# Performance work log

Measured on AMD Instinct MI355X. Metric: run time of the kernel, lower is better.

## Reference

```python
import jax, jax.numpy as jnp
import numpy as np

WS = 8       # window_size
SHIFT = 4    # shift_size
NH = 6       # num_heads
C = 192      # dim
EPS = 1e-5


def _rel_index(ws):
    # standard Swin relative position index, [ws*ws, ws*ws]
    coords = np.stack(np.meshgrid(np.arange(ws), np.arange(ws), indexing='ij')).reshape(2, -1)
    rel = coords[:, :, None] - coords[:, None, :]            # [2, N, N]
    rel = rel.transpose(1, 2, 0) + (ws - 1)                  # shift to >= 0
    return rel[..., 0] * (2 * ws - 1) + rel[..., 1]          # [N, N]


def _attn_mask(h, w, ws, shift):
    # shifted-window attention mask, [nW, N, N] with 0 / -100
    img = np.zeros((h, w), dtype=np.float32)
    cnt = 0
    for hs in (slice(0, -ws), slice(-ws, -shift), slice(-shift, None)):
        for wsl in (slice(0, -ws), slice(-ws, -shift), slice(-shift, None)):
            img[hs, wsl] = cnt
            cnt += 1
    mw = img.reshape(h // ws, ws, w // ws, ws).transpose(0, 2, 1, 3).reshape(-1, ws * ws)
    diff = mw[:, None, :] - mw[:, :, None]
    return np.where(diff != 0, -100.0, 0.0).astype(np.float32)


def _ln(x, g, b):
    m = x.mean(-1, keepdims=True)
    v = ((x - m) ** 2).mean(-1, keepdims=True)
    return (x - m) / jnp.sqrt(v + EPS) * g + b


def setup_inputs() -> dict:
    key = jax.random.key(0)
    ks = jax.random.split(key, 16)
    B, H, W = 32, 64, 64
    Ch = 4 * C
    s = 0.02
    return {
        'x': jax.random.normal(ks[0], (B, H * W, C), jnp.float32),
        'h': H,
        'w': W,
        'norm1_g': jnp.ones((C,), jnp.float32),
        'norm1_b': jnp.zeros((C,), jnp.float32),
        'qkv_w': jax.random.normal(ks[1], (3 * C, C), jnp.float32) * s,
        'qkv_b': jnp.zeros((3 * C,), jnp.float32),
        'rpb_table': jax.random.normal(ks[2], ((2 * WS - 1) ** 2, NH), jnp.float32) * s,
        'proj_w': jax.random.normal(ks[3], (C, C), jnp.float32) * s,
        'proj_b': jnp.zeros((C,), jnp.float32),
        'norm2_g': jnp.ones((C,), jnp.float32),
        'norm2_b': jnp.zeros((C,), jnp.float32),
        'fc1_w': jax.random.normal(ks[4], (Ch, C), jnp.float32) * s,
        'fc1_b': jnp.zeros((Ch,), jnp.float32),
        'fc2_w': jax.random.normal(ks[5], (C, Ch), jnp.float32) * s,
        'fc2_b': jnp.zeros((C,), jnp.float32),
    }


def reference(x, h, w, norm1_g, norm1_b, qkv_w, qkv_b, rpb_table, proj_w, proj_b,
              norm2_g, norm2_b, fc1_w, fc1_b, fc2_w, fc2_b):
    B, L, _ = x.shape
    N = WS * WS
    hd = C // NH
    scale = hd ** -0.5
    nW = (h // WS) * (w // WS)

    shortcut = x
    xn = _ln(x, norm1_g, norm1_b).reshape(B, h, w, C)
    xs = jnp.roll(xn, (-SHIFT, -SHIFT), (1, 2))
    # window partition -> [B*nW, N, C]
    xw = xs.reshape(B, h // WS, WS, w // WS, WS, C).transpose(0, 1, 3, 2, 4, 5).reshape(-1, N, C)

    qkv = (xw @ qkv_w.T + qkv_b).reshape(-1, N, 3, NH, hd).transpose(2, 0, 3, 1, 4)
    q, k, v = qkv[0], qkv[1], qkv[2]                          # [B*nW, NH, N, hd]
    attn = jnp.einsum('whnd,whmd->whnm', q * scale, k)        # [B*nW, NH, N, N]
    bias = rpb_table[jnp.asarray(_rel_index(WS))].transpose(2, 0, 1)  # [NH, N, N]
    attn = attn + bias[None]
    mask = jnp.asarray(_attn_mask(h, w, WS, SHIFT))           # [nW, N, N]
    attn = attn.reshape(B, nW, NH, N, N) + mask[None, :, None]
    attn = jax.nn.softmax(attn.reshape(-1, NH, N, N), axis=-1)
    out = jnp.einsum('whnm,whmd->whnd', attn, v).transpose(0, 2, 1, 3).reshape(-1, N, C)
    out = out @ proj_w.T + proj_b

    # window reverse + unroll
    out = out.reshape(B, h // WS, w // WS, WS, WS, C).transpose(0, 1, 3, 2, 4, 5).reshape(B, h, w, C)
    out = jnp.roll(out, (SHIFT, SHIFT), (1, 2)).reshape(B, h * w, C)

    x = shortcut + out
    xn = _ln(x, norm2_g, norm2_b)
    mlp = jax.nn.gelu(xn @ fc1_w.T + fc1_b, approximate=False) @ fc2_w.T + fc2_b
    return x + mlp
```

## Files before the change

### kernel.cpp

```cpp
#include <hip/hip_runtime.h>
#include <hip/hip_bf16.h>
#include <math.h>

typedef __bf16 bf16;
typedef __bf16 bf16x8 __attribute__((ext_vector_type(8)));
typedef float f32x4 __attribute__((ext_vector_type(4)));

typedef const __attribute__((address_space(1))) char gchar;
typedef __attribute__((address_space(3))) char lchar;

#define BATCH 32
#define HW 64
#define L 4096
#define CDIM 192
#define NHEADS 6
#define HD 32
#define NTOK 131072
#define QKVC 576
#define CH 768

template <bool PERM, typename TIN>
__global__ __launch_bounds__(256) void ln_kernel(const TIN* __restrict__ xin,
                                                 const float* __restrict__ g,
                                                 const float* __restrict__ bta,
                                                 bf16* __restrict__ yout) {
  int wave = threadIdx.x >> 6;
  int lane = threadIdx.x & 63;
  int tok = blockIdx.x * 4 + wave;
  int src;
  if (PERM) {
    int win = tok >> 6;
    int n = tok & 63;
    int bb = win >> 6;
    int wid = win & 63;
    int i = ((wid >> 3) << 3) + (n >> 3);
    int j = ((wid & 7) << 3) + (n & 7);
    int sh = (i + 4) & 63;
    int sw = (j + 4) & 63;
    src = bb * L + sh * HW + sw;
  } else {
    src = tok;
  }
  const TIN* sp = xin + (size_t)src * CDIM;
  float v0 = (float)sp[lane];
  float v1 = (float)sp[lane + 64];
  float v2 = (float)sp[lane + 128];
  float s = v0 + v1 + v2;
#pragma unroll
  for (int off = 32; off; off >>= 1) s += __shfl_xor(s, off, 64);
  float mean = s * (1.0f / 192.0f);
  float d0 = v0 - mean, d1 = v1 - mean, d2 = v2 - mean;
  float q = d0 * d0 + d1 * d1 + d2 * d2;
#pragma unroll
  for (int off = 32; off; off >>= 1) q += __shfl_xor(q, off, 64);
  float rstd = rsqrtf(q * (1.0f / 192.0f) + 1e-5f);
  bf16* dp = yout + (size_t)tok * CDIM;
  dp[lane]       = (bf16)(d0 * rstd * g[lane]       + bta[lane]);
  dp[lane + 64]  = (bf16)(d1 * rstd * g[lane + 64]  + bta[lane + 64]);
  dp[lane + 128] = (bf16)(d2 * rstd * g[lane + 128] + bta[lane + 128]);
}

template <int EPI, typename TR, typename TO>
__global__ __launch_bounds__(256) void gemm_bt(const bf16* __restrict__ A,
                                               const float* __restrict__ W,
                                               const float* __restrict__ bias,
                                               const TR* __restrict__ res,
                                               TO* __restrict__ Cout,
                                               int M, int N, int K, int ldw) {
  __shared__ alignas(16) bf16 As[128 * 32];
  __shared__ alignas(16) bf16 Bs[64 * 32];
  const int gx = gridDim.x;
  const int nb = gx * gridDim.y;
  const int id = blockIdx.y * gx + blockIdx.x;
  const int per = nb >> 3;
  const int jj = ((id & 7) * per) + (id >> 3);
  const int n0 = (jj % gx) * 64;
  const int m0 = (jj / gx) * 128;
  const int tid = threadIdx.x;
  const int lane = tid & 63;
  const int wave = tid >> 6;
  const int wm = (wave >> 1) * 64;
  const int wn = (wave & 1) * 32;
  const int lr = lane & 15;
  const int quad = lane >> 4;

  f32x4 acc[4][2];
#pragma unroll
  for (int i = 0; i < 4; i++)
#pragma unroll
    for (int j = 0; j < 2; j++) acc[i][j] = (f32x4){0.f, 0.f, 0.f, 0.f};

  const int arow = tid >> 2;
  const int akq = (tid & 3) * 8;

  for (int k0 = 0; k0 < K; k0 += 32) {
    const bf16* Ap = A + (size_t)(m0 + arow) * K + k0 + akq;
    *(uint4*)(&As[arow * 32 + akq]) = *(const uint4*)Ap;
    *(uint4*)(&As[(arow + 64) * 32 + akq]) = *(const uint4*)(Ap + (size_t)64 * K);
    const float* Wp = W + (size_t)(n0 + arow) * ldw + k0 + akq;
    float4 w0 = *(const float4*)Wp;
    float4 w1 = *(const float4*)(Wp + 4);
    bf16x8 bw;
    bw[0] = (bf16)w0.x; bw[1] = (bf16)w0.y; bw[2] = (bf16)w0.z; bw[3] = (bf16)w0.w;
    bw[4] = (bf16)w1.x; bw[5] = (bf16)w1.y; bw[6] = (bf16)w1.z; bw[7] = (bf16)w1.w;
    *(bf16x8*)(&Bs[arow * 32 + akq]) = bw;
    __syncthreads();

    bf16x8 af[4], bfr[2];
#pragma unroll
    for (int mi = 0; mi < 4; mi++)
      af[mi] = *(const bf16x8*)(&As[(wm + mi * 16 + lr) * 32 + quad * 8]);
#pragma unroll
    for (int nj = 0; nj < 2; nj++)
      bfr[nj] = *(const bf16x8*)(&Bs[(wn + nj * 16 + lr) * 32 + quad * 8]);
#pragma unroll
    for (int mi = 0; mi < 4; mi++)
#pragma unroll
      for (int nj = 0; nj < 2; nj++)
        acc[mi][nj] = __builtin_amdgcn_mfma_f32_16x16x32_bf16(af[mi], bfr[nj],
                                                              acc[mi][nj], 0, 0, 0);
    __syncthreads();
  }

#pragma unroll
  for (int mi = 0; mi < 4; mi++) {
#pragma unroll
    for (int nj = 0; nj < 2; nj++) {
      int col = n0 + wn + nj * 16 + lr;
      float bv = bias[col];
#pragma unroll
      for (int r = 0; r < 4; r++) {
        int row = m0 + wm + mi * 16 + quad * 4 + r;
        float v = acc[mi][nj][r] + bv;
        size_t didx;
        if (EPI == 3) {
          int win = row >> 6, n = row & 63;
          int bb = win >> 6, wid = win & 63;
          int i = ((wid >> 3) << 3) + (n >> 3);
          int j = ((wid & 7) << 3) + (n & 7);
          int fi = (i + 4) & 63;
          int fj = (j + 4) & 63;
          didx = ((size_t)(bb * L + fi * HW + fj)) * (size_t)N + col;
          v += (float)res[didx];
        } else {
          didx = (size_t)row * N + col;
        }
        Cout[didx] = (TO)v;
      }
    }
  }
}

__device__ __forceinline__ int region64(int h) {
  return (h < 56) ? 0 : ((h < 60) ? 1 : 2);
}

__global__ __launch_bounds__(64) void attn_kernel(const bf16* __restrict__ qkv,
                                                  const float* __restrict__ rpb,
                                                  bf16* __restrict__ out) {
  __shared__ alignas(16) bf16 QKP[64 * 64];
  __shared__ alignas(16) bf16 Vt[32 * 64];
  bf16* Qs = QKP;
  bf16* Ks = QKP + 64 * 32;
  bf16* Ps = QKP;
  const int win = blockIdx.x;
  const int head = blockIdx.y;
  const int lane = threadIdx.x;
  const int lr = lane & 15;
  const int quad = lane >> 4;
  const int wid = win & 63;
  const int wi = wid >> 3, wj = wid & 7;

  const bf16* base = qkv + (size_t)win * 64 * QKVC + head * HD;
#pragma unroll
  for (int rep = 0; rep < 4; rep++) {
    int r = (lane >> 2) + rep * 16;
    int c = (lane & 3) * 8;
    *(uint4*)(&Qs[r * 32 + c]) = *(const uint4*)(base + (size_t)r * QKVC + c);
    *(uint4*)(&Ks[r * 32 + c]) = *(const uint4*)(base + CDIM + (size_t)r * QKVC + c);
    uint4 vv = *(const uint4*)(base + 2 * CDIM + (size_t)r * QKVC + c);
    bf16x8 v8 = __builtin_bit_cast(bf16x8, vv);
#pragma unroll
    for (int j = 0; j < 8; j++) Vt[(c + j) * 64 + r] = v8[j];
  }
  __syncthreads();

  f32x4 s[4][4];
  {
    bf16x8 qf[4], kf[4];
#pragma unroll
    for (int mi = 0; mi < 4; mi++)
      qf[mi] = *(const bf16x8*)(&Qs[(mi * 16 + lr) * 32 + quad * 8]);
#pragma unroll
    for (int nj = 0; nj < 4; nj++)
      kf[nj] = *(const bf16x8*)(&Ks[(nj * 16 + lr) * 32 + quad * 8]);
#pragma unroll
    for (int mi = 0; mi < 4; mi++)
#pragma unroll
      for (int nj = 0; nj < 4; nj++)
        s[mi][nj] = __builtin_amdgcn_mfma_f32_16x16x32_bf16(
            qf[mi], kf[nj], (f32x4){0.f, 0.f, 0.f, 0.f}, 0, 0, 0);
  }

  const float scale = 0.17677669529663687f;
#pragma unroll
  for (int mi = 0; mi < 4; mi++) {
#pragma unroll
    for (int nj = 0; nj < 4; nj++) {
#pragma unroll
      for (int r = 0; r < 4; r++) {
        int rr = mi * 16 + quad * 4 + r;
        int cc = nj * 16 + lr;
        int qi = rr >> 3, qj = rr & 7, ki = cc >> 3, kj = cc & 7;
        int idx = (qi - ki + 7) * 15 + (qj - kj + 7);
        float bv = rpb[idx * NHEADS + head];
        int regr = 3 * region64(wi * 8 + qi) + region64(wj * 8 + qj);
        int regc = 3 * region64(wi * 8 + ki) + region64(wj * 8 + kj);
        float mv = (regr != regc) ? -100.0f : 0.0f;
        s[mi][nj][r] = s[mi][nj][r] * scale + bv + mv;
      }
    }
  }

#pragma unroll
  for (int mi = 0; mi < 4; mi++) {
#pragma unroll
    for (int r = 0; r < 4; r++) {
      float mx = s[mi][0][r];
#pragma unroll
      for (int nj = 1; nj < 4; nj++) mx = fmaxf(mx, s[mi][nj][r]);
#pragma unroll
      for (int off = 1; off < 16; off <<= 1) mx = fmaxf(mx, __shfl_xor(mx, off, 64));
      float sum = 0.f;
#pragma unroll
      for (int nj = 0; nj < 4; nj++) {
        float p = __expf(s[mi][nj][r] - mx);
        s[mi][nj][r] = p;
        sum += p;
      }
#pragma unroll
      for (int off = 1; off < 16; off <<= 1) sum += __shfl_xor(sum, off, 64);
      float inv = 1.0f / sum;
#pragma unroll
      for (int nj = 0; nj < 4; nj++) s[mi][nj][r] *= inv;
    }
  }

#pragma unroll
  for (int mi = 0; mi < 4; mi++)
#pragma unroll
    for (int nj = 0; nj < 4; nj++)
#pragma unroll
      for (int r = 0; r < 4; r++)
        Ps[(mi * 16 + quad * 4 + r) * 64 + nj * 16 + lr] = (bf16)s[mi][nj][r];
  __syncthreads();

  f32x4 o[4][2];
#pragma unroll
  for (int mi = 0; mi < 4; mi++)
#pragma unroll
    for (int nj = 0; nj < 2; nj++) o[mi][nj] = (f32x4){0.f, 0.f, 0.f, 0.f};
#pragma unroll
  for (int ks = 0; ks < 2; ks++) {
    bf16x8 pf[4], vf[2];
#pragma unroll
    for (int mi = 0; mi < 4; mi++)
      pf[mi] = *(const bf16x8*)(&Ps[(mi * 16 + lr) * 64 + ks * 32 + quad * 8]);
#pragma unroll
    for (int nj = 0; nj < 2; nj++)
      vf[nj] = *(const bf16x8*)(&Vt[(nj * 16 + lr) * 64 + ks * 32 + quad * 8]);
#pragma unroll
    for (int mi = 0; mi < 4; mi++)
#pragma unroll
      for (int nj = 0; nj < 2; nj++)
        o[mi][nj] = __builtin_amdgcn_mfma_f32_16x16x32_bf16(pf[mi], vf[nj],
                                                            o[mi][nj], 0, 0, 0);
  }

#pragma unroll
  for (int mi = 0; mi < 4; mi++)
#pragma unroll
    for (int nj = 0; nj < 2; nj++)
#pragma unroll
      for (int r = 0; r < 4; r++) {
        size_t row = (size_t)win * 64 + mi * 16 + quad * 4 + r;
        int col = head * HD + nj * 16 + lr;
        out[row * CDIM + col] = (bf16)o[mi][nj][r];
      }
}

__global__ __launch_bounds__(256) void wconv_kernel(const float* __restrict__ fc1w,
                                                    const float* __restrict__ fc2w,
                                                    bf16* __restrict__ W1b,
                                                    bf16* __restrict__ W2b) {
  int i = blockIdx.x * 256 + threadIdx.x;
  {
    int h = i / 192;
    int cc = i - h * 192;
    int gs = cc >> 3, e = cc & 7;
    int g = (gs & ~7) | ((gs & 7) ^ (h & 7));
    W1b[i] = (bf16)fc1w[h * 192 + g * 8 + e];
  }
  {
    int c = i / 12288;
    int rem = i - c * 12288;
    int n = rem >> 6;
    int cc = rem & 63;
    int gs = cc >> 3, e = cc & 7;
    int g = gs ^ (n & 7);
    W2b[i] = (bf16)fc2w[n * 768 + c * 64 + g * 8 + e];
  }
}

__global__ __launch_bounds__(512, 4) void mlp_fused(
    const bf16* __restrict__ X1,
    const float* __restrict__ g2,
    const float* __restrict__ bt2,
    const bf16* __restrict__ W1b,
    const bf16* __restrict__ W2b,
    const float* __restrict__ b1,
    const float* __restrict__ b2,
    float* __restrict__ out) {
  __shared__ alignas(16) bf16 W1s[64 * 192];
  __shared__ alignas(16) bf16 W2s[192 * 64];
  __shared__ alignas(16) bf16 Hs[8][16 * 64];
  __shared__ float Gs[192], Bn[192];

  const int tid = threadIdx.x;
  const int lane = tid & 63;
  const int wave = tid >> 6;
  const int lr = lane & 15;
  const int quad = lane >> 4;
  const int m0 = blockIdx.x * 128;
  const int arow = m0 + wave * 16 + lr;

  if (tid < 192) { Gs[tid] = g2[tid]; Bn[tid] = bt2[tid]; }
  __syncthreads();

  bf16x8 xr[6];
  {
    const bf16* xp = X1 + (size_t)arow * CDIM + quad * 8;
#pragma unroll
    for (int ks = 0; ks < 6; ks++) xr[ks] = *(const bf16x8*)(xp + ks * 32);
  }
  float s1 = 0.f, s2 = 0.f;
#pragma unroll
  for (int ks = 0; ks < 6; ks++)
#pragma unroll
    for (int j = 0; j < 8; j++) {
      float v = (float)xr[ks][j];
      s1 += v;
      s2 = fmaf(v, v, s2);
    }
  s1 += __shfl_xor(s1, 16, 64); s1 += __shfl_xor(s1, 32, 64);
  s2 += __shfl_xor(s2, 16, 64); s2 += __shfl_xor(s2, 32, 64);
  float mean = s1 * (1.0f / 192.0f);
  float var = fmaxf(s2 * (1.0f / 192.0f) - mean * mean, 0.0f);
  float rstd = rsqrtf(var + 1e-5f);
  bf16x8 aF[6];
#pragma unroll
  for (int ks = 0; ks < 6; ks++) {
    int cb = ks * 32 + quad * 8;
    bf16x8 a;
#pragma unroll
    for (int j = 0; j < 8; j++)
      a[j] = (bf16)(((float)xr[ks][j] - mean) * rstd * Gs[cb + j] + Bn[cb + j]);
    aF[ks] = a;
  }

  f32x4 oacc[12];
#pragma unroll
  for (int nt = 0; nt < 12; nt++) oacc[nt] = (f32x4){0.f, 0.f, 0.f, 0.f};

  for (int c = 0; c < 12; c++) {
    const int h0 = c * 64;
    {
      const size_t cb = (size_t)c * 24576;
      const int off = wave * 1024 + lane * 16;
      const char* g1 = (const char*)W1b + cb + off;
      const char* gg2 = (const char*)W2b + cb + off;
      char* l1 = (char*)W1s + wave * 1024;
      char* l2 = (char*)W2s + wave * 1024;
#pragma unroll
      for (int i = 0; i < 3; i++) {
        __builtin_amdgcn_global_load_lds((gchar*)(g1 + i * 8192),
                                         (lchar*)(l1 + i * 8192), 16, 0, 0);
        __builtin_amdgcn_global_load_lds((gchar*)(gg2 + i * 8192),
                                         (lchar*)(l2 + i * 8192), 16, 0, 0);
      }
    }
    __syncthreads();

    f32x4 hacc[4];
#pragma unroll
    for (int nj = 0; nj < 4; nj++) hacc[nj] = (f32x4){0.f, 0.f, 0.f, 0.f};
#pragma unroll
    for (int ks = 0; ks < 6; ks++) {
      int c8 = ks * 4 + quad;
      int base = (c8 & ~7) | ((c8 & 7) ^ (lr & 7));
#pragma unroll
      for (int nj = 0; nj < 4; nj++) {
        bf16x8 bF = *(const bf16x8*)(&W1s[(nj * 16 + lr) * 192 + base * 8]);
        hacc[nj] = __builtin_amdgcn_mfma_f32_16x16x32_bf16(aF[ks], bF, hacc[nj], 0, 0, 0);
      }
    }

#pragma unroll
    for (int nj = 0; nj < 4; nj++) {
      float bh = b1[h0 + nj * 16 + lr];
#pragma unroll
      for (int r = 0; r < 4; r++) {
        float h = hacc[nj][r] + bh;
        float x = fabsf(h) * 0.70710678118654752f;
        float t = __fdividef(1.0f, fmaf(0.3275911f, x, 1.0f));
        float p = t * (0.254829592f +
                  t * (-0.284496736f +
                  t * (1.421413741f +
                  t * (-1.453152027f + t * 1.061405429f))));
        float er = fmaf(-p, __expf(-x * x), 1.0f);
        er = copysignf(er, h);
        float gl = 0.5f * h * (1.0f + er);
        int hr = quad * 4 + r;
        int col = nj * 16 + lr;
        int c8 = col >> 3;
        int c8s = c8 ^ (hr & 7);
        Hs[wave][hr * 64 + c8s * 8 + (col & 7)] = (bf16)gl;
      }
    }

#pragma unroll
    for (int ks = 0; ks < 2; ks++) {
      int c8 = ks * 4 + quad;
      int c8s = c8 ^ (lr & 7);
      bf16x8 hF = *(const bf16x8*)(&Hs[wave][lr * 64 + c8s * 8]);
#pragma unroll
      for (int nt = 0; nt < 12; nt++) {
        bf16x8 wF = *(const bf16x8*)(&W2s[(nt * 16 + lr) * 64 + c8s * 8]);
        oacc[nt] = __builtin_amdgcn_mfma_f32_16x16x32_bf16(hF, wF, oacc[nt], 0, 0, 0);
      }
    }
    __syncthreads();
  }

#pragma unroll
  for (int nt = 0; nt < 12; nt++) {
    float fb = b2[nt * 16 + lr];
#pragma unroll
    for (int r = 0; r < 4; r++) {
      size_t row = (size_t)(m0 + wave * 16 + quad * 4 + r);
      size_t idx = row * CDIM + nt * 16 + lr;
      out[idx] = oacc[nt][r] + fb + (float)X1[idx];
    }
  }
}

extern "C" void kernel_launch(void* const* d_in, const int* in_sizes, int n_in,
                              void* d_out, int out_size, void* d_ws, size_t ws_size,
                              hipStream_t stream) {
  const float* x      = (const float*)d_in[0];
  const float* n1g    = (const float*)d_in[3];
  const float* n1b    = (const float*)d_in[4];
  const float* qkv_w  = (const float*)d_in[5];
  const float* qkv_b  = (const float*)d_in[6];
  const float* rpb    = (const float*)d_in[7];
  const float* proj_w = (const float*)d_in[8];
  const float* proj_b = (const float*)d_in[9];
  const float* n2g    = (const float*)d_in[10];
  const float* n2b    = (const float*)d_in[11];
  const float* fc1_w  = (const float*)d_in[12];
  const float* fc1_b  = (const float*)d_in[13];
  const float* fc2_w  = (const float*)d_in[14];
  const float* fc2_b  = (const float*)d_in[15];
  float* out = (float*)d_out;

  char* wsb = (char*)d_ws;
  bf16* Q   = (bf16*)wsb;
  bf16* X1  = (bf16*)wsb;
  bf16* W1b = (bf16*)(wsb + 52428800ull);
  bf16* W2b = (bf16*)(wsb + 52428800ull + 294912ull);
  bf16* T   = (bf16*)(wsb + 150994944ull);

  ln_kernel<true, float><<<32768, 256, 0, stream>>>(x, n1g, n1b, T);
  gemm_bt<0, float, bf16><<<dim3(9, 1024), 256, 0, stream>>>(
      T, qkv_w, qkv_b, nullptr, Q, NTOK, QKVC, CDIM, CDIM);
  attn_kernel<<<dim3(2048, 6), 64, 0, stream>>>(Q, rpb, T);
  gemm_bt<3, float, bf16><<<dim3(3, 1024), 256, 0, stream>>>(
      T, proj_w, proj_b, x, X1, NTOK, CDIM, CDIM, CDIM);
  wconv_kernel<<<576, 256, 0, stream>>>(fc1_w, fc2_w, W1b, W2b);
  mlp_fused<<<1024, 512, 0, stream>>>(X1, n2g, n2b, W1b, W2b, fc1_b, fc2_b, out);
}
```

Measured before the change: 537.5 us.

## Fuse LayerNorm1 with shifted-window gather into QKV GEMM; vectorize MLP hidden stores

Removes the standalone LN1 kernel. The QKV GEMM now computes per-row mean and rstd from the rolled, window-partitioned fp32 input and normalizes while staging A tiles into LDS, which avoids writing and re-reading a bf16 normalized intermediate. Each of the 9 column blocks recomputes the LN statistics and re-reads the fp32 input rows, so input traffic goes up. Separately, the MLP's first MFMA swaps its operands so each lane holds 4 consecutive hidden columns, giving vectorized bias loads and packed bf16x4 stores into the swizzled Hs buffer.

```diff
diff --git a/kernel.cpp b/kernel.cpp
--- a/kernel.cpp
+++ b/kernel.cpp
@@ -3,6 +3,7 @@
 #include <math.h>
 
 typedef __bf16 bf16;
+typedef __bf16 bf16x4 __attribute__((ext_vector_type(4)));
 typedef __bf16 bf16x8 __attribute__((ext_vector_type(8)));
 typedef float f32x4 __attribute__((ext_vector_type(4)));
 
@@ -19,45 +20,146 @@
 #define QKVC 576
 #define CH 768
 
-template <bool PERM, typename TIN>
-__global__ __launch_bounds__(256) void ln_kernel(const TIN* __restrict__ xin,
-                                                 const float* __restrict__ g,
-                                                 const float* __restrict__ bta,
-                                                 bf16* __restrict__ yout) {
-  int wave = threadIdx.x >> 6;
-  int lane = threadIdx.x & 63;
-  int tok = blockIdx.x * 4 + wave;
-  int src;
-  if (PERM) {
-    int win = tok >> 6;
-    int n = tok & 63;
-    int bb = win >> 6;
-    int wid = win & 63;
-    int i = ((wid >> 3) << 3) + (n >> 3);
-    int j = ((wid & 7) << 3) + (n & 7);
-    int sh = (i + 4) & 63;
-    int sw = (j + 4) & 63;
-    src = bb * L + sh * HW + sw;
-  } else {
-    src = tok;
-  }
-  const TIN* sp = xin + (size_t)src * CDIM;
-  float v0 = (float)sp[lane];
-  float v1 = (float)sp[lane + 64];
-  float v2 = (float)sp[lane + 128];
-  float s = v0 + v1 + v2;
-#pragma unroll
-  for (int off = 32; off; off >>= 1) s += __shfl_xor(s, off, 64);
-  float mean = s * (1.0f / 192.0f);
-  float d0 = v0 - mean, d1 = v1 - mean, d2 = v2 - mean;
-  float q = d0 * d0 + d1 * d1 + d2 * d2;
-#pragma unroll
-  for (int off = 32; off; off >>= 1) q += __shfl_xor(q, off, 64);
-  float rstd = rsqrtf(q * (1.0f / 192.0f) + 1e-5f);
-  bf16* dp = yout + (size_t)tok * CDIM;
-  dp[lane]       = (bf16)(d0 * rstd * g[lane]       + bta[lane]);
-  dp[lane + 64]  = (bf16)(d1 * rstd * g[lane + 64]  + bta[lane + 64]);
-  dp[lane + 128] = (bf16)(d2 * rstd * g[lane + 128] + bta[lane + 128]);
+__device__ __forceinline__ int srcrow_of(int row) {
+  int win = row >> 6, n = row & 63;
+  int bb = win >> 6, wid = win & 63;
+  int i = ((wid >> 3) << 3) + (n >> 3);
+  int j = ((wid & 7) << 3) + (n & 7);
+  return bb * L + ((i + 4) & 63) * HW + ((j + 4) & 63);
+}
+
+__global__ __launch_bounds__(256) void gemm_ln_qkv(
+    const float* __restrict__ X,
+    const float* __restrict__ g1,
+    const float* __restrict__ bt1,
+    const float* __restrict__ W,
+    const float* __restrict__ bias,
+    bf16* __restrict__ Cout) {
+  __shared__ alignas(16) bf16 As[128 * 32];
+  __shared__ alignas(16) bf16 Bs[64 * 32];
+  __shared__ float MuS[128], RsS[128];
+  const int gx = gridDim.x;
+  const int nb = gx * gridDim.y;
+  const int id = blockIdx.y * gx + blockIdx.x;
+  const int per = nb >> 3;
+  const int jj = ((id & 7) * per) + (id >> 3);
+  const int n0 = (jj % gx) * 64;
+  const int m0 = (jj / gx) * 128;
+  const int tid = threadIdx.x;
+  const int lane = tid & 63;
+  const int wave = tid >> 6;
+  const int wm = (wave >> 1) * 64;
+  const int wn = (wave & 1) * 32;
+  const int lr = lane & 15;
+  const int quad = lane >> 4;
+
+  {
+    int row = tid >> 1, half = tid & 1;
+    const float* xp = X + (size_t)srcrow_of(m0 + row) * CDIM + half * 96;
+    float s1 = 0.f, s2 = 0.f;
+#pragma unroll
+    for (int i = 0; i < 24; i++) {
+      float4 v = *(const float4*)(xp + i * 4);
+      s1 += v.x + v.y + v.z + v.w;
+      s2 = fmaf(v.x, v.x, fmaf(v.y, v.y, fmaf(v.z, v.z, fmaf(v.w, v.w, s2))));
+    }
+    s1 += __shfl_xor(s1, 1, 64);
+    s2 += __shfl_xor(s2, 1, 64);
+    if (!half) {
+      float mean = s1 * (1.0f / 192.0f);
+      float var = fmaxf(s2 * (1.0f / 192.0f) - mean * mean, 0.0f);
+      MuS[row] = mean;
+      RsS[row] = rsqrtf(var + 1e-5f);
+    }
+  }
+  __syncthreads();
+
+  f32x4 acc[4][2];
+#pragma unroll
+  for (int i = 0; i < 4; i++)
+#pragma unroll
+    for (int j = 0; j < 2; j++) acc[i][j] = (f32x4){0.f, 0.f, 0.f, 0.f};
+
+  const int arow = tid >> 2;
+  const int akq = (tid & 3) * 8;
+  const size_t sa = (size_t)srcrow_of(m0 + arow) * CDIM;
+  const size_t sb = (size_t)srcrow_of(m0 + arow + 64) * CDIM;
+
+  for (int k0 = 0; k0 < CDIM; k0 += 32) {
+    float4 ga = *(const float4*)(g1 + k0 + akq);
+    float4 gb = *(const float4*)(g1 + k0 + akq + 4);
+    float4 ba = *(const float4*)(bt1 + k0 + akq);
+    float4 bb = *(const float4*)(bt1 + k0 + akq + 4);
+    {
+      float4 v0 = *(const float4*)(X + sa + k0 + akq);
+      float4 v1 = *(const float4*)(X + sa + k0 + akq + 4);
+      float mu = MuS[arow], rs = RsS[arow];
+      bf16x8 p;
+      p[0] = (bf16)((v0.x - mu) * rs * ga.x + ba.x);
+      p[1] = (bf16)((v0.y - mu) * rs * ga.y + ba.y);
+      p[2] = (bf16)((v0.z - mu) * rs * ga.z + ba.z);
+      p[3] = (bf16)((v0.w - mu) * rs * ga.w + ba.w);
+      p[4] = (bf16)((v1.x - mu) * rs * gb.x + bb.x);
+      p[5] = (bf16)((v1.y - mu) * rs * gb.y + bb.y);
+      p[6] = (bf16)((v1.z - mu) * rs * gb.z + bb.z);
+      p[7] = (bf16)((v1.w - mu) * rs * gb.w + bb.w);
+      *(bf16x8*)(&As[arow * 32 + akq]) = p;
+    }
+    {
+      float4 v0 = *(const float4*)(X + sb + k0 + akq);
+      float4 v1 = *(const float4*)(X + sb + k0 + akq + 4);
+      float mu = MuS[arow + 64], rs = RsS[arow + 64];
+      bf16x8 p;
+      p[0] = (bf16)((v0.x - mu) * rs * ga.x + ba.x);
+      p[1] = (bf16)((v0.y - mu) * rs * ga.y + ba.y);
+      p[2] = (bf16)((v0.z - mu) * rs * ga.z + ba.z);
+      p[3] = (bf16)((v0.w - mu) * rs * ga.w + ba.w);
+      p[4] = (bf16)((v1.x - mu) * rs * gb.x + bb.x);
+      p[5] = (bf16)((v1.y - mu) * rs * gb.y + bb.y);
+      p[6] = (bf16)((v1.z - mu) * rs * gb.z + bb.z);
+      p[7] = (bf16)((v1.w - mu) * rs * gb.w + bb.w);
+      *(bf16x8*)(&As[(arow + 64) * 32 + akq]) = p;
+    }
+    {
+      const float* Wp = W + (size_t)(n0 + arow) * CDIM + k0 + akq;
+      float4 w0 = *(const float4*)Wp;
+      float4 w1 = *(const float4*)(Wp + 4);
+      bf16x8 bw;
+      bw[0] = (bf16)w0.x; bw[1] = (bf16)w0.y; bw[2] = (bf16)w0.z; bw[3] = (bf16)w0.w;
+      bw[4] = (bf16)w1.x; bw[5] = (bf16)w1.y; bw[6] = (bf16)w1.z; bw[7] = (bf16)w1.w;
+      *(bf16x8*)(&Bs[arow * 32 + akq]) = bw;
+    }
+    __syncthreads();
+
+    bf16x8 af[4], bfr[2];
+#pragma unroll
+    for (int mi = 0; mi < 4; mi++)
+      af[mi] = *(const bf16x8*)(&As[(wm + mi * 16 + lr) * 32 + quad * 8]);
+#pragma unroll
+    for (int nj = 0; nj < 2; nj++)
+      bfr[nj] = *(const bf16x8*)(&Bs[(wn + nj * 16 + lr) * 32 + quad * 8]);
+#pragma unroll
+    for (int mi = 0; mi < 4; mi++)
+#pragma unroll
+      for (int nj = 0; nj < 2; nj++)
+        acc[mi][nj] = __builtin_amdgcn_mfma_f32_16x16x32_bf16(af[mi], bfr[nj],
+                                                              acc[mi][nj], 0, 0, 0);
+    __syncthreads();
+  }
+
+#pragma unroll
+  for (int mi = 0; mi < 4; mi++) {
+#pragma unroll
+    for (int nj = 0; nj < 2; nj++) {
+      int col = n0 + wn + nj * 16 + lr;
+      float bv = bias[col];
+#pragma unroll
+      for (int r = 0; r < 4; r++) {
+        int row = m0 + wm + mi * 16 + quad * 4 + r;
+        Cout[(size_t)row * QKVC + col] = (bf16)(acc[mi][nj][r] + bv);
+      }
+    }
+  }
 }
 
 template <int EPI, typename TR, typename TO>
@@ -134,13 +236,7 @@
         float v = acc[mi][nj][r] + bv;
         size_t didx;
         if (EPI == 3) {
-          int win = row >> 6, n = row & 63;
-          int bb = win >> 6, wid = win & 63;
-          int i = ((wid >> 3) << 3) + (n >> 3);
-          int j = ((wid & 7) << 3) + (n & 7);
-          int fi = (i + 4) & 63;
-          int fj = (j + 4) & 63;
-          didx = ((size_t)(bb * L + fi * HW + fj)) * (size_t)N + col;
+          didx = ((size_t)srcrow_of(row)) * (size_t)N + col;
           v += (float)res[didx];
         } else {
           didx = (size_t)row * N + col;
@@ -377,15 +473,15 @@
     {
       const size_t cb = (size_t)c * 24576;
       const int off = wave * 1024 + lane * 16;
-      const char* g1 = (const char*)W1b + cb + off;
-      const char* gg2 = (const char*)W2b + cb + off;
+      const char* gp1 = (const char*)W1b + cb + off;
+      const char* gp2 = (const char*)W2b + cb + off;
       char* l1 = (char*)W1s + wave * 1024;
       char* l2 = (char*)W2s + wave * 1024;
 #pragma unroll
       for (int i = 0; i < 3; i++) {
-        __builtin_amdgcn_global_load_lds((gchar*)(g1 + i * 8192),
+        __builtin_amdgcn_global_load_lds((gchar*)(gp1 + i * 8192),
                                          (lchar*)(l1 + i * 8192), 16, 0, 0);
-        __builtin_amdgcn_global_load_lds((gchar*)(gg2 + i * 8192),
+        __builtin_amdgcn_global_load_lds((gchar*)(gp2 + i * 8192),
                                          (lchar*)(l2 + i * 8192), 16, 0, 0);
       }
     }
@@ -393,24 +489,26 @@
 
     f32x4 hacc[4];
 #pragma unroll
-    for (int nj = 0; nj < 4; nj++) hacc[nj] = (f32x4){0.f, 0.f, 0.f, 0.f};
+    for (int hj = 0; hj < 4; hj++) hacc[hj] = (f32x4){0.f, 0.f, 0.f, 0.f};
 #pragma unroll
     for (int ks = 0; ks < 6; ks++) {
       int c8 = ks * 4 + quad;
       int base = (c8 & ~7) | ((c8 & 7) ^ (lr & 7));
 #pragma unroll
-      for (int nj = 0; nj < 4; nj++) {
-        bf16x8 bF = *(const bf16x8*)(&W1s[(nj * 16 + lr) * 192 + base * 8]);
-        hacc[nj] = __builtin_amdgcn_mfma_f32_16x16x32_bf16(aF[ks], bF, hacc[nj], 0, 0, 0);
-      }
-    }
-
-#pragma unroll
-    for (int nj = 0; nj < 4; nj++) {
-      float bh = b1[h0 + nj * 16 + lr];
+      for (int hj = 0; hj < 4; hj++) {
+        bf16x8 wf = *(const bf16x8*)(&W1s[(hj * 16 + lr) * 192 + base * 8]);
+        hacc[hj] = __builtin_amdgcn_mfma_f32_16x16x32_bf16(wf, aF[ks], hacc[hj], 0, 0, 0);
+      }
+    }
+
+#pragma unroll
+    for (int hj = 0; hj < 4; hj++) {
+      float4 bh4 = *(const float4*)(&b1[h0 + hj * 16 + quad * 4]);
+      float bhv[4] = {bh4.x, bh4.y, bh4.z, bh4.w};
+      bf16x4 pk;
 #pragma unroll
       for (int r = 0; r < 4; r++) {
-        float h = hacc[nj][r] + bh;
+        float h = hacc[hj][r] + bhv[r];
         float x = fabsf(h) * 0.70710678118654752f;
         float t = __fdividef(1.0f, fmaf(0.3275911f, x, 1.0f));
         float p = t * (0.254829592f +
@@ -419,20 +517,18 @@
                   t * (-1.453152027f + t * 1.061405429f))));
         float er = fmaf(-p, __expf(-x * x), 1.0f);
         er = copysignf(er, h);
-        float gl = 0.5f * h * (1.0f + er);
-        int hr = quad * 4 + r;
-        int col = nj * 16 + lr;
-        int c8 = col >> 3;
-        int c8s = c8 ^ (hr & 7);
-        Hs[wave][hr * 64 + c8s * 8 + (col & 7)] = (bf16)gl;
-      }
+        pk[r] = (bf16)(0.5f * h * (1.0f + er));
+      }
+      int gw = (hj * 4 + quad) ^ ((lr & 7) << 1);
+      *(bf16x4*)(&Hs[wave][lr * 64 + gw * 4]) = pk;
     }
 
 #pragma unroll
     for (int ks = 0; ks < 2; ks++) {
+      int gr = (ks * 8 + quad * 2) ^ ((lr & 7) << 1);
+      bf16x8 hF = *(const bf16x8*)(&Hs[wave][lr * 64 + gr * 4]);
       int c8 = ks * 4 + quad;
       int c8s = c8 ^ (lr & 7);
-      bf16x8 hF = *(const bf16x8*)(&Hs[wave][lr * 64 + c8s * 8]);
 #pragma unroll
       for (int nt = 0; nt < 12; nt++) {
         bf16x8 wF = *(const bf16x8*)(&W2s[(nt * 16 + lr) * 64 + c8s * 8]);
@@ -480,9 +576,7 @@
   bf16* W2b = (bf16*)(wsb + 52428800ull + 294912ull);
   bf16* T   = (bf16*)(wsb + 150994944ull);
 
-  ln_kernel<true, float><<<32768, 256, 0, stream>>>(x, n1g, n1b, T);
-  gemm_bt<0, float, bf16><<<dim3(9, 1024), 256, 0, stream>>>(
-      T, qkv_w, qkv_b, nullptr, Q, NTOK, QKVC, CDIM, CDIM);
+  gemm_ln_qkv<<<dim3(9, 1024), 256, 0, stream>>>(x, n1g, n1b, qkv_w, qkv_b, Q);
   attn_kernel<<<dim3(2048, 6), 64, 0, stream>>>(Q, rpb, T);
   gemm_bt<3, float, bf16><<<dim3(3, 1024), 256, 0, stream>>>(
       T, proj_w, proj_b, x, X1, NTOK, CDIM, CDIM, CDIM);
```

Result: slower. 652.8 us (+21.4%).
